# Performance work log

Hardware: AMD Instinct MI355X
Metric: run time of the kernel (lower is better)

Reference implementation:

```python
import jax, jax.numpy as jnp
import numpy as np

E, TOP, C, H, W, B = 8, 2, 128, 96, 96, 8
NUM_GATES = 4
KH = 3  # capsule conv kernel


def setup_inputs() -> dict:
    key = jax.random.key(0)
    ks = jax.random.split(key, 6)
    x = jax.random.normal(ks[0], (B, C, H, W), jnp.float32)
    # xavier_uniform for gates: bound = sqrt(6/(fan_in+fan_out))
    bound = float(np.sqrt(6.0 / (C + E)))
    G = jax.random.uniform(ks[1], (NUM_GATES, C, E), jnp.float32, -bound, bound)
    # per-expert capsule convs: the 16 parallel (C->capsule_dim) 3x3 convs are
    # stacked along the output-channel axis into one (C->C) conv per expert
    Wc = jax.random.normal(ks[2], (E, C, C, KH, KH), jnp.float32) * (1.0 / np.sqrt(C * KH * KH))
    bc = jax.random.normal(ks[3], (E, C), jnp.float32) * 0.01
    # 1x1 output projection per expert
    Wp = jax.random.normal(ks[4], (E, C, C), jnp.float32) * (1.0 / np.sqrt(C))
    bp = jax.random.normal(ks[5], (E, C), jnp.float32) * 0.01
    return {"x": x, "G": G, "Wc": Wc, "bc": bc, "Wp": Wp, "bp": bp}


def _squash(u):
    # squash over the full channel dim (dim=1), matching the torch module
    sn = jnp.sum(u * u, axis=1, keepdims=True)
    return (sn / (1.0 + sn)) * u / jnp.sqrt(sn + 1e-8)


def _expert(x, wc, bc, wp, bp):
    u = jax.lax.conv_general_dilated(
        x, wc, window_strides=(1, 1), padding='SAME',
        dimension_numbers=('NCHW', 'OIHW', 'NCHW')) + bc[None, :, None, None]
    u = jax.nn.relu(u)
    u = _squash(u)
    return jnp.einsum('bchw,oc->bohw', u, wp) + bp[None, :, None, None]


def _cv_squared(v):
    v = v.astype(jnp.float32)
    return jnp.var(v, ddof=1) / (jnp.mean(v) ** 2 + 1e-10)


def reference(x, G, Wc, bc, Wp, bp):
    Bn = x.shape[0]
    # run every expert on the full batch (dense equivalent of the masked dispatch)
    y_all = jax.vmap(lambda wc_, bc_, wp_, bp_: _expert(x, wc_, bc_, wp_, bp_))(
        Wc, bc, Wp, bp)  # [E, B, C, H, W]
    x_gap = jnp.mean(x, axis=(2, 3))  # [B, C]  (adaptive avg pool to 1x1)
    ys, losses = [], []
    for g in range(NUM_GATES):
        probs = jax.nn.softmax(x_gap @ G[g], axis=1)           # [B, E]
        tv, ti = jax.lax.top_k(probs, TOP)                     # [B, TOP]
        tw = jax.nn.softmax(tv, axis=1)                        # renormalized top-k weights
        out = jnp.zeros_like(x)
        for k in range(TOP):
            y_sel = y_all[ti[:, k], jnp.arange(Bn)]            # gather per-sample expert out
            out = out + y_sel * tw[:, k][:, None, None, None]
        ys.append(out)
        losses.append(_cv_squared(jnp.sum(probs, axis=0)))     # cv^2 of expert usage
    total_loss = jnp.mean(jnp.stack(losses))
    return (*ys, total_loss)
```

## Files before the change

kernel.cpp:

```cpp
#include <hip/hip_runtime.h>
#include <math.h>

#define CHW 9216
#define OPG 9437184

typedef unsigned short u16;
typedef __attribute__((ext_vector_type(8))) short short8;
typedef __attribute__((ext_vector_type(4))) float f32x4;

#define WS_XT  8192
#define WS_AT  18882560
#define WS_WPT 21241856

__device__ __forceinline__ u16 f2bf(float f) {
    unsigned u = __float_as_uint(f);
    u += 0x7fff + ((u >> 16) & 1);
    return (u16)(u >> 16);
}

__device__ __forceinline__ void gload_lds16(const void* g, void* l) {
    __builtin_amdgcn_global_load_lds(
        (const __attribute__((address_space(1))) void*)g,
        (__attribute__((address_space(3))) void*)l, 16, 0, 0);
}

__global__ void gap_kernel(const float* __restrict__ x, float* __restrict__ xgap) {
    int bc = blockIdx.x;
    const float* p = x + (size_t)bc * CHW;
    float s = 0.f;
    for (int i = threadIdx.x; i < CHW; i += 256) s += p[i];
    __shared__ float red[256];
    red[threadIdx.x] = s;
    __syncthreads();
    for (int off = 128; off > 0; off >>= 1) {
        if (threadIdx.x < off) red[threadIdx.x] += red[threadIdx.x + off];
        __syncthreads();
    }
    if (threadIdx.x == 0) xgap[bc] = red[0] * (1.0f / 9216.0f);
}

__global__ void gate_kernel(const float* __restrict__ G, float* __restrict__ ws,
                            float* __restrict__ loss_out) {
    __shared__ float gap_s[1024];
    __shared__ float logits[64];
    __shared__ float probs[64];
    __shared__ float vsum[8];
    __shared__ float losses[4];
    int t = threadIdx.x;
    for (int i = t; i < 1024; i += 64) gap_s[i] = ws[i];
    int b = t >> 3, e = t & 7;
    int* iw = (int*)(ws + 1344);
    float* wt = ws + 1408;
    __syncthreads();
    for (int g = 0; g < 4; ++g) {
        float acc = 0.f;
        const float* Gg = G + g * 1024;
        for (int c = 0; c < 128; ++c) acc += gap_s[b * 128 + c] * Gg[c * 8 + e];
        logits[t] = acc;
        __syncthreads();
        float m = -1e30f;
        for (int j = 0; j < 8; ++j) m = fmaxf(m, logits[b * 8 + j]);
        float den = 0.f;
        for (int j = 0; j < 8; ++j) den += expf(logits[b * 8 + j] - m);
        float pr = expf(acc - m) / den;
        probs[t] = pr;
        __syncthreads();
        if (e == 0) {
            int i0 = 0; float v0 = probs[b * 8];
            for (int j = 1; j < 8; ++j) { float v = probs[b * 8 + j]; if (v > v0) { v0 = v; i0 = j; } }
            int i1 = -1; float v1 = -1e30f;
            for (int j = 0; j < 8; ++j) { if (j == i0) continue; float v = probs[b * 8 + j]; if (v > v1) { v1 = v; i1 = j; } }
            float r = expf(v1 - v0);
            float inv = 1.f / (1.f + r);
            iw[g * 16 + b * 2 + 0] = i0;
            iw[g * 16 + b * 2 + 1] = i1;
            wt[g * 16 + b * 2 + 0] = inv;
            wt[g * 16 + b * 2 + 1] = r * inv;
        }
        if (t < 8) {
            float v = 0.f;
            for (int bb = 0; bb < 8; ++bb) v += probs[bb * 8 + t];
            vsum[t] = v;
        }
        __syncthreads();
        if (t == 0) {
            float mean = 0.f;
            for (int j = 0; j < 8; ++j) mean += vsum[j];
            mean *= 0.125f;
            float var = 0.f;
            for (int j = 0; j < 8; ++j) { float d = vsum[j] - mean; var += d * d; }
            var *= (1.f / 7.f);
            losses[g] = var / (mean * mean + 1e-10f);
        }
        __syncthreads();
    }
    if (t == 0) loss_out[0] = 0.25f * (losses[0] + losses[1] + losses[2] + losses[3]);
}

__global__ void pre_x(const float* __restrict__ x, u16* __restrict__ Xt) {
    int h = blockIdx.x, b = blockIdx.y, t = threadIdx.x;
    __shared__ u16 lds[12288];
    const float* xb = x + ((size_t)b * 128) * CHW + h * 96;
    for (int i = t; i < 12288; i += 256) {
        int c = i / 96, w = i - c * 96;
        lds[(c >> 6) * 6144 + w * 64 + ((c & 63) ^ ((w & 7) << 3))] = f2bf(xb[(size_t)c * CHW + w]);
    }
    __syncthreads();
    const unsigned* l32 = (const unsigned*)lds;
    unsigned* o32 = (unsigned*)Xt;
    for (int i = t; i < 6144; i += 256) {
        int hf = (i >= 3072) ? 1 : 0;
        int rem = i - hf * 3072;
        o32[((size_t)(b * 2 + hf) * 96 + h) * 3072 + rem] = l32[i];
    }
}

__global__ void pre_wc2(const float* __restrict__ Wc, u16* __restrict__ At2) {
    int idx = blockIdx.x * 256 + threadIdx.x;
    int s = idx & 7;
    int lane = (idx >> 3) & 63;
    int mb = (idx >> 9) & 3;
    int mi = (idx >> 11) & 1;
    int ck = (idx >> 12) & 1;
    int rem = idx >> 13;
    int r = rem % 9;
    int rem2 = rem / 9;
    int hf = rem2 & 1;
    int e = rem2 >> 1;
    int l15 = lane & 15, quad = lane >> 4;
    int o = mi * 64 + mb * 16 + l15;
    int cin = hf * 64 + ck * 32 + quad * 8 + s;
    size_t src = (((size_t)e * 128 + o) * 128 + cin) * 9 + r;
    At2[idx] = f2bf(Wc[src]);
}

__global__ void pre_wp(const float* __restrict__ Wp, u16* __restrict__ Wpt) {
    int i = blockIdx.x * 256 + threadIdx.x;
    if (i < 131072) Wpt[i] = f2bf(Wp[i]);
}

__launch_bounds__(512, 2)
__global__ void expert_kernel(const u16* __restrict__ Xt, const u16* __restrict__ At2,
                              const u16* __restrict__ Wpt,
                              const float* __restrict__ bc, const float* __restrict__ bp,
                              const float* __restrict__ ws, float* __restrict__ out) {
    int hs = blockIdx.x, b = blockIdx.y, g = blockIdx.z;
    int h0 = hs * 2;
    int t = threadIdx.x, lane = t & 63, wv = t >> 6;
    int mi = wv & 1, ni = wv >> 1;
    int l15 = lane & 15, quad = lane >> 4, q8 = quad * 8;
    int nrow = ni >> 1;
    int ncb = (ni & 1) * 48;

    const int* iw = (const int*)(ws + 1344);
    const float* wt = ws + 1408;
    int ee[2];
    float wwt[2];
    ee[0] = iw[g * 16 + b * 2 + 0]; ee[1] = iw[g * 16 + b * 2 + 1];
    wwt[0] = wt[g * 16 + b * 2 + 0]; wwt[1] = wt[g * 16 + b * 2 + 1];

    __shared__ __align__(16) char smem[115712];
    u16* Hs = (u16*)smem;
    float* part_s = (float*)smem;
    u16* v_s = (u16*)(smem + 9216);

    f32x4 zero = {0.f, 0.f, 0.f, 0.f};
    f32x4 acc[2][12];
    #pragma unroll
    for (int i = 0; i < 12; ++i) { acc[0][i] = zero; acc[1][i] = zero; }

    const u16* Ab0 = At2 + (size_t)(ee[0] * 2) * 73728;
    const u16* Ab1 = At2 + (size_t)(ee[1] * 2) * 73728;

    #define ASRC(P, U) ((P) + ((U) >= 18 ? 73728 + ((U) - 18) * 4096 : (U) * 4096))
    #define STAGE(U) { u16* ab_ = (u16*)(smem + 50176 + ((U) & 3) * 16384);          \
                       gload_lds16(ASRC(Ab0, (U)) + t * 8, ab_ + t * 8);             \
                       gload_lds16(ASRC(Ab1, (U)) + t * 8, ab_ + 4096 + t * 8); }

    {
        uint4 z; z.x = z.y = z.z = z.w = 0u;
        #pragma unroll
        for (int rr = 0; rr < 4; ++rr) {
            int row = h0 - 1 + rr;
            if (row < 0 || row >= 96)
                for (int i = t; i < 784; i += 512) *(uint4*)(Hs + rr * 6272 + i * 8) = z;
        }
        if (t < 64) {
            int rr = t >> 4, cs = (t >> 3) & 1, p = t & 7;
            *(uint4*)(Hs + rr * 6272 + cs * 97 * 64 + p * 8) = z;
        }
        const u16* Xb = Xt + (size_t)(b * 2 + 0) * 96 * 6144;
        #pragma unroll
        for (int rr = 0; rr < 4; ++rr) {
            int row = h0 - 1 + rr;
            if (row >= 0 && row < 96) {
                const u16* src = Xb + (size_t)row * 6144;
                u16* dst = Hs + rr * 6272 + 64;
                for (int i = t; i < 768; i += 512) gload_lds16(src + i * 8, dst + i * 8);
            }
        }
    }
    STAGE(0); STAGE(1);
    __syncthreads();

    #pragma unroll
    for (int u = 0; u < 36; ++u) {
        if (u == 18) {
            __builtin_amdgcn_s_barrier();
            const u16* Xb = Xt + (size_t)(b * 2 + 1) * 96 * 6144;
            #pragma unroll
            for (int rr = 0; rr < 4; ++rr) {
                int row = h0 - 1 + rr;
                if (row >= 0 && row < 96) {
                    const u16* src = Xb + (size_t)row * 6144;
                    u16* dst = Hs + rr * 6272 + 64;
                    for (int i = t; i < 768; i += 512) gload_lds16(src + i * 8, dst + i * 8);
                }
            }
        }
        if (u <= 33) STAGE(u + 2);
        if (u == 18 || u == 35) asm volatile("s_waitcnt vmcnt(0)" ::: "memory");
        else if (u == 34)       asm volatile("s_waitcnt vmcnt(2)" ::: "memory");
        else                    asm volatile("s_waitcnt vmcnt(4)" ::: "memory");
        __builtin_amdgcn_s_barrier();

        int s = (u >= 18) ? u - 18 : u;
        int r = s >> 1, ck = s & 1;
        int dyi = r / 3, dxi = r - dyi * 3;
        const u16* ab = (const u16*)(smem + 50176 + (u & 3) * 16384);

        short8 af0[4], af1[4], bv[3];
        #pragma unroll
        for (int mb = 0; mb < 4; ++mb) {
            af0[mb] = *(const short8*)(ab + mi * 2048 + mb * 512 + lane * 8);
            af1[mb] = *(const short8*)(ab + 4096 + mi * 2048 + mb * 512 + lane * 8);
        }
        int hb = (nrow + dyi) * 12544;
        #pragma unroll
        for (int j = 0; j < 3; ++j) {
            int col = ncb + j * 16 + l15 + dxi;
            int ba = hb + col * 128 + ((q8 ^ (((col - 1) & 7) << 3)) << 1);
            bv[j] = *(const short8*)(smem + (ba ^ (ck << 6)));
        }
        __builtin_amdgcn_s_setprio(1);
        #pragma unroll
        for (int mb = 0; mb < 4; ++mb)
            #pragma unroll
            for (int j = 0; j < 3; ++j) {
                acc[0][mb * 3 + j] = __builtin_amdgcn_mfma_f32_16x16x32_bf16(af0[mb], bv[j], acc[0][mb * 3 + j], 0, 0, 0);
                acc[1][mb * 3 + j] = __builtin_amdgcn_mfma_f32_16x16x32_bf16(af1[mb], bv[j], acc[1][mb * 3 + j], 0, 0, 0);
            }
        __builtin_amdgcn_s_setprio(0);
    }
    #undef STAGE
    #undef ASRC

    #pragma unroll
    for (int xp = 0; xp < 2; ++xp) {
        int e_ = ee[xp];
        __syncthreads();
        #pragma unroll
        for (int j = 0; j < 3; ++j) {
            int n = ni * 48 + j * 16 + l15;
            float ssum = 0.f;
            #pragma unroll
            for (int mb = 0; mb < 4; ++mb) {
                f32x4 a = acc[xp][mb * 3 + j];
                #pragma unroll
                for (int rg = 0; rg < 4; ++rg) {
                    float u = fmaxf(a[rg] + bc[e_ * 128 + mi * 64 + mb * 16 + quad * 4 + rg], 0.f);
                    a[rg] = u; ssum += u * u;
                }
                acc[xp][mb * 3 + j] = a;
            }
            part_s[n * 12 + mi * 4 + quad] = ssum;
        }
        __syncthreads();
        #pragma unroll
        for (int j = 0; j < 3; ++j) {
            int n = ni * 48 + j * 16 + l15;
            f32x4 p0 = *(const f32x4*)(part_s + n * 12);
            f32x4 p1 = *(const f32x4*)(part_s + n * 12 + 4);
            float sn2 = p0[0] + p0[1] + p0[2] + p0[3] + p1[0] + p1[1] + p1[2] + p1[3];
            float fsj = sn2 / ((1.f + sn2) * sqrtf(sn2 + 1e-8f));
            int sw = (n & 7) << 3;
            #pragma unroll
            for (int mb = 0; mb < 4; ++mb) {
                f32x4 a = acc[xp][mb * 3 + j];
                short4 pk;
                pk.x = (short)f2bf(a[0] * fsj); pk.y = (short)f2bf(a[1] * fsj);
                pk.z = (short)f2bf(a[2] * fsj); pk.w = (short)f2bf(a[3] * fsj);
                int cb = mb * 16 + quad * 4;
                *(short4*)(v_s + n * 128 + ((cb ^ sw) | (mi << 6))) = pk;
            }
        }
        __syncthreads();
        #pragma unroll
        for (int i = 0; i < 12; ++i) acc[xp][i] = zero;
        const u16* We_ = Wpt + (size_t)e_ * 16384;
        #pragma unroll
        for (int kk = 0; kk < 4; ++kk) {
            short8 af[4];
            #pragma unroll
            for (int mb = 0; mb < 4; ++mb)
                af[mb] = *(const short8*)(We_ + (mi * 64 + mb * 16 + l15) * 128 + kk * 32 + q8);
            short8 bvv[3];
            #pragma unroll
            for (int j = 0; j < 3; ++j) {
                int n = ni * 48 + j * 16 + l15;
                int sw = (n & 7) << 3;
                int pos = ((kk & 2) << 5) | ((((kk & 1) << 5) + q8) ^ sw);
                bvv[j] = *(const short8*)(v_s + n * 128 + pos);
            }
            #pragma unroll
            for (int mb = 0; mb < 4; ++mb)
                #pragma unroll
                for (int j = 0; j < 3; ++j)
                    acc[xp][mb * 3 + j] = __builtin_amdgcn_mfma_f32_16x16x32_bf16(af[mb], bvv[j], acc[xp][mb * 3 + j], 0, 0, 0);
        }
    }

    int row = h0 + nrow;
    #pragma unroll
    for (int mb = 0; mb < 4; ++mb)
        #pragma unroll
        for (int rg = 0; rg < 4; ++rg) {
            int o = mi * 64 + mb * 16 + quad * 4 + rg;
            float y0b = bp[ee[0] * 128 + o];
            float y1b = bp[ee[1] * 128 + o];
            size_t obase = (size_t)g * OPG + ((size_t)(b * 128 + o)) * CHW + (size_t)row * 96;
            #pragma unroll
            for (int j = 0; j < 3; ++j) {
                float y0 = acc[0][mb * 3 + j][rg] + y0b;
                float y1 = acc[1][mb * 3 + j][rg] + y1b;
                out[obase + ncb + j * 16 + l15] = wwt[0] * y0 + wwt[1] * y1;
            }
        }
}

extern "C" void kernel_launch(void* const* d_in, const int* in_sizes, int n_in,
                              void* d_out, int out_size, void* d_ws, size_t ws_size,
                              hipStream_t stream) {
    const float* x  = (const float*)d_in[0];
    const float* G  = (const float*)d_in[1];
    const float* Wc = (const float*)d_in[2];
    const float* bc = (const float*)d_in[3];
    const float* Wp = (const float*)d_in[4];
    const float* bp = (const float*)d_in[5];
    float* out = (float*)d_out;
    float* ws  = (float*)d_ws;
    u16* Xt  = (u16*)((char*)d_ws + WS_XT);
    u16* At2 = (u16*)((char*)d_ws + WS_AT);
    u16* Wpt = (u16*)((char*)d_ws + WS_WPT);

    gap_kernel<<<dim3(1024), dim3(256), 0, stream>>>(x, ws);
    gate_kernel<<<dim3(1), dim3(64), 0, stream>>>(G, ws, out + (size_t)4 * OPG);
    pre_x<<<dim3(96, 8), dim3(256), 0, stream>>>(x, Xt);
    pre_wc2<<<dim3(4608), dim3(256), 0, stream>>>(Wc, At2);
    pre_wp<<<dim3(512), dim3(256), 0, stream>>>(Wp, Wpt);
    expert_kernel<<<dim3(48, 8, 4), dim3(512), 0, stream>>>(Xt, At2, Wpt, bc, bp, ws, out);
}
```

Before: 429.7 us.

## Prefetch A fragments into registers one step ahead with triple-buffered LDS

Cuts the LDS staging ring for expert weight tiles from four buffers to three. Each step now loads the next step's A fragments into a double-buffered register array, so the MFMAs use fragments already held in registers. Synchronisation moves to a full vmcnt(0) wait plus barrier at the end of every iteration. The aim is to hide LDS read latency behind MFMA work, at the cost of more VGPRs and less in-flight global-load depth, since the wait now drains all loads each step.

```diff
diff --git a/kernel.cpp b/kernel.cpp
--- a/kernel.cpp
+++ b/kernel.cpp
@@ -159,7 +159,7 @@
     ee[0] = iw[g * 16 + b * 2 + 0]; ee[1] = iw[g * 16 + b * 2 + 1];
     wwt[0] = wt[g * 16 + b * 2 + 0]; wwt[1] = wt[g * 16 + b * 2 + 1];
 
-    __shared__ __align__(16) char smem[115712];
+    __shared__ __align__(16) char smem[99328];
     u16* Hs = (u16*)smem;
     float* part_s = (float*)smem;
     u16* v_s = (u16*)(smem + 9216);
@@ -169,11 +169,13 @@
     #pragma unroll
     for (int i = 0; i < 12; ++i) { acc[0][i] = zero; acc[1][i] = zero; }
 
+    int abase = mi * 2048 + lane * 8;
+
     const u16* Ab0 = At2 + (size_t)(ee[0] * 2) * 73728;
     const u16* Ab1 = At2 + (size_t)(ee[1] * 2) * 73728;
 
     #define ASRC(P, U) ((P) + ((U) >= 18 ? 73728 + ((U) - 18) * 4096 : (U) * 4096))
-    #define STAGE(U) { u16* ab_ = (u16*)(smem + 50176 + ((U) & 3) * 16384);          \
+    #define STAGE(U) { u16* ab_ = (u16*)(smem + 50176 + ((U) % 3) * 16384);          \
                        gload_lds16(ASRC(Ab0, (U)) + t * 8, ab_ + t * 8);             \
                        gload_lds16(ASRC(Ab1, (U)) + t * 8, ab_ + 4096 + t * 8); }
 
@@ -203,10 +205,19 @@
     STAGE(0); STAGE(1);
     __syncthreads();
 
+    short8 afr[2][2][4];
+    {
+        const u16* ab = (const u16*)(smem + 50176);
+        #pragma unroll
+        for (int mb = 0; mb < 4; ++mb) {
+            afr[0][0][mb] = *(const short8*)(ab + abase + mb * 512);
+            afr[0][1][mb] = *(const short8*)(ab + 4096 + abase + mb * 512);
+        }
+    }
+
     #pragma unroll
     for (int u = 0; u < 36; ++u) {
         if (u == 18) {
-            __builtin_amdgcn_s_barrier();
             const u16* Xb = Xt + (size_t)(b * 2 + 1) * 96 * 6144;
             #pragma unroll
             for (int rr = 0; rr < 4; ++rr) {
@@ -217,40 +228,42 @@
                     for (int i = t; i < 768; i += 512) gload_lds16(src + i * 8, dst + i * 8);
                 }
             }
-        }
-        if (u <= 33) STAGE(u + 2);
-        if (u == 18 || u == 35) asm volatile("s_waitcnt vmcnt(0)" ::: "memory");
-        else if (u == 34)       asm volatile("s_waitcnt vmcnt(2)" ::: "memory");
-        else                    asm volatile("s_waitcnt vmcnt(4)" ::: "memory");
-        __builtin_amdgcn_s_barrier();
+            asm volatile("s_waitcnt vmcnt(0)" ::: "memory");
+            __builtin_amdgcn_s_barrier();
+        }
+        if (u < 34) STAGE(u + 2);
 
         int s = (u >= 18) ? u - 18 : u;
         int r = s >> 1, ck = s & 1;
         int dyi = r / 3, dxi = r - dyi * 3;
-        const u16* ab = (const u16*)(smem + 50176 + (u & 3) * 16384);
-
-        short8 af0[4], af1[4], bv[3];
-        #pragma unroll
-        for (int mb = 0; mb < 4; ++mb) {
-            af0[mb] = *(const short8*)(ab + mi * 2048 + mb * 512 + lane * 8);
-            af1[mb] = *(const short8*)(ab + 4096 + mi * 2048 + mb * 512 + lane * 8);
-        }
         int hb = (nrow + dyi) * 12544;
+
+        short8 bv[3];
         #pragma unroll
         for (int j = 0; j < 3; ++j) {
             int col = ncb + j * 16 + l15 + dxi;
             int ba = hb + col * 128 + ((q8 ^ (((col - 1) & 7) << 3)) << 1);
             bv[j] = *(const short8*)(smem + (ba ^ (ck << 6)));
         }
+        if (u < 35) {
+            const u16* ab = (const u16*)(smem + 50176 + ((u + 1) % 3) * 16384);
+            #pragma unroll
+            for (int mb = 0; mb < 4; ++mb) {
+                afr[(u + 1) & 1][0][mb] = *(const short8*)(ab + abase + mb * 512);
+                afr[(u + 1) & 1][1][mb] = *(const short8*)(ab + 4096 + abase + mb * 512);
+            }
+        }
         __builtin_amdgcn_s_setprio(1);
         #pragma unroll
         for (int mb = 0; mb < 4; ++mb)
             #pragma unroll
             for (int j = 0; j < 3; ++j) {
-                acc[0][mb * 3 + j] = __builtin_amdgcn_mfma_f32_16x16x32_bf16(af0[mb], bv[j], acc[0][mb * 3 + j], 0, 0, 0);
-                acc[1][mb * 3 + j] = __builtin_amdgcn_mfma_f32_16x16x32_bf16(af1[mb], bv[j], acc[1][mb * 3 + j], 0, 0, 0);
+                acc[0][mb * 3 + j] = __builtin_amdgcn_mfma_f32_16x16x32_bf16(afr[u & 1][0][mb], bv[j], acc[0][mb * 3 + j], 0, 0, 0);
+                acc[1][mb * 3 + j] = __builtin_amdgcn_mfma_f32_16x16x32_bf16(afr[u & 1][1][mb], bv[j], acc[1][mb * 3 + j], 0, 0, 0);
             }
         __builtin_amdgcn_s_setprio(0);
+        asm volatile("s_waitcnt vmcnt(0)" ::: "memory");
+        __builtin_amdgcn_s_barrier();
     }
     #undef STAGE
     #undef ASRC
```

After: 450.5 us. 1.05x slower.

## Software-pipeline LDS fragment reads with MFMA in conv main loop, triple-buffer A

Applied to the files above, without the earlier changes.

Restructures the 36-step conv K loop into two halves with register double-buffered B fragments and split A fragment reads. Reads for the next step are interleaved between the two expert MFMA groups. The A staging ring shrinks from four to three LDS buffers, cutting shared memory use. The intent is to hide LDS read latency behind MFMA work and possibly raise occupancy, at the cost of more registers and two barriers per step. Each step also waits on vmcnt(0) for global loads.

```diff
diff --git a/kernel.cpp b/kernel.cpp
--- a/kernel.cpp
+++ b/kernel.cpp
@@ -159,7 +159,7 @@
     ee[0] = iw[g * 16 + b * 2 + 0]; ee[1] = iw[g * 16 + b * 2 + 1];
     wwt[0] = wt[g * 16 + b * 2 + 0]; wwt[1] = wt[g * 16 + b * 2 + 1];
 
-    __shared__ __align__(16) char smem[115712];
+    __shared__ __align__(16) char smem[99328];
     u16* Hs = (u16*)smem;
     float* part_s = (float*)smem;
     u16* v_s = (u16*)(smem + 9216);
@@ -169,13 +169,26 @@
     #pragma unroll
     for (int i = 0; i < 12; ++i) { acc[0][i] = zero; acc[1][i] = zero; }
 
+    int abase = mi * 2048 + lane * 8;
+
     const u16* Ab0 = At2 + (size_t)(ee[0] * 2) * 73728;
     const u16* Ab1 = At2 + (size_t)(ee[1] * 2) * 73728;
 
     #define ASRC(P, U) ((P) + ((U) >= 18 ? 73728 + ((U) - 18) * 4096 : (U) * 4096))
-    #define STAGE(U) { u16* ab_ = (u16*)(smem + 50176 + ((U) & 3) * 16384);          \
+    #define STAGE(U) { u16* ab_ = (u16*)(smem + 50176 + ((U) % 3) * 16384);          \
                        gload_lds16(ASRC(Ab0, (U)) + t * 8, ab_ + t * 8);             \
                        gload_lds16(ASRC(Ab1, (U)) + t * 8, ab_ + 4096 + t * 8); }
+    #define RD_AF(DST, G, XOFF) { const u16* abr_ = (const u16*)(smem + 50176 + ((G) % 3) * 16384) + (XOFF); \
+        _Pragma("unroll") for (int mb_ = 0; mb_ < 4; ++mb_) DST[mb_] = *(const short8*)(abr_ + abase + mb_ * 512); }
+    #define RD_BV(DST, G) { const int s_ = (G) % 18, r_ = s_ >> 1, ck_ = s_ & 1;     \
+        const int dyi_ = r_ / 3, dxi_ = r_ - dyi_ * 3, hb_ = (nrow + dyi_) * 12544;  \
+        _Pragma("unroll") for (int j_ = 0; j_ < 3; ++j_) {                           \
+            int col_ = ncb + j_ * 16 + l15 + dxi_;                                   \
+            int ba_ = hb_ + col_ * 128 + ((q8 ^ (((col_ - 1) & 7) << 3)) << 1);      \
+            DST[j_] = *(const short8*)(smem + (ba_ ^ (ck_ << 6))); } }
+    #define MFMA12(XP, AF, BV) { _Pragma("unroll") for (int mb_ = 0; mb_ < 4; ++mb_) \
+        _Pragma("unroll") for (int j_ = 0; j_ < 3; ++j_)                             \
+            acc[XP][mb_ * 3 + j_] = __builtin_amdgcn_mfma_f32_16x16x32_bf16(AF[mb_], BV[j_], acc[XP][mb_ * 3 + j_], 0, 0, 0); }
 
     {
         uint4 z; z.x = z.y = z.z = z.w = 0u;
@@ -203,10 +216,11 @@
     STAGE(0); STAGE(1);
     __syncthreads();
 
+    short8 af0[4], af1[4], bvA[3], bvB[3];
+
     #pragma unroll
-    for (int u = 0; u < 36; ++u) {
-        if (u == 18) {
-            __builtin_amdgcn_s_barrier();
+    for (int hf = 0; hf < 2; ++hf) {
+        if (hf == 1) {
             const u16* Xb = Xt + (size_t)(b * 2 + 1) * 96 * 6144;
             #pragma unroll
             for (int rr = 0; rr < 4; ++rr) {
@@ -217,43 +231,38 @@
                     for (int i = t; i < 768; i += 512) gload_lds16(src + i * 8, dst + i * 8);
                 }
             }
-        }
-        if (u <= 33) STAGE(u + 2);
-        if (u == 18 || u == 35) asm volatile("s_waitcnt vmcnt(0)" ::: "memory");
-        else if (u == 34)       asm volatile("s_waitcnt vmcnt(2)" ::: "memory");
-        else                    asm volatile("s_waitcnt vmcnt(4)" ::: "memory");
-        __builtin_amdgcn_s_barrier();
-
-        int s = (u >= 18) ? u - 18 : u;
-        int r = s >> 1, ck = s & 1;
-        int dyi = r / 3, dxi = r - dyi * 3;
-        const u16* ab = (const u16*)(smem + 50176 + (u & 3) * 16384);
-
-        short8 af0[4], af1[4], bv[3];
-        #pragma unroll
-        for (int mb = 0; mb < 4; ++mb) {
-            af0[mb] = *(const short8*)(ab + mi * 2048 + mb * 512 + lane * 8);
-            af1[mb] = *(const short8*)(ab + 4096 + mi * 2048 + mb * 512 + lane * 8);
-        }
-        int hb = (nrow + dyi) * 12544;
-        #pragma unroll
-        for (int j = 0; j < 3; ++j) {
-            int col = ncb + j * 16 + l15 + dxi;
-            int ba = hb + col * 128 + ((q8 ^ (((col - 1) & 7) << 3)) << 1);
-            bv[j] = *(const short8*)(smem + (ba ^ (ck << 6)));
-        }
-        __builtin_amdgcn_s_setprio(1);
-        #pragma unroll
-        for (int mb = 0; mb < 4; ++mb)
-            #pragma unroll
-            for (int j = 0; j < 3; ++j) {
-                acc[0][mb * 3 + j] = __builtin_amdgcn_mfma_f32_16x16x32_bf16(af0[mb], bv[j], acc[0][mb * 3 + j], 0, 0, 0);
-                acc[1][mb * 3 + j] = __builtin_amdgcn_mfma_f32_16x16x32_bf16(af1[mb], bv[j], acc[1][mb * 3 + j], 0, 0, 0);
-            }
-        __builtin_amdgcn_s_setprio(0);
+            asm volatile("s_waitcnt vmcnt(0)" ::: "memory");
+            __builtin_amdgcn_s_barrier();
+        }
+        RD_AF(af0, hf * 18, 0);
+        RD_BV(bvA, hf * 18);
+
+        #pragma unroll
+        for (int u = 0; u < 18; ++u) {
+            const int gg = hf * 18 + u;
+            if (gg + 2 <= 35) STAGE(gg + 2);
+            RD_AF(af1, gg, 4096);
+            __builtin_amdgcn_s_setprio(1);
+            if (u & 1) { MFMA12(0, af0, bvB); } else { MFMA12(0, af0, bvA); }
+            __builtin_amdgcn_s_setprio(0);
+            __builtin_amdgcn_s_barrier();
+            if (u < 17) {
+                if (u & 1) { RD_BV(bvA, gg + 1); } else { RD_BV(bvB, gg + 1); }
+                RD_AF(af0, gg + 1, 0);
+            }
+            __builtin_amdgcn_s_setprio(1);
+            if (u & 1) { MFMA12(1, af1, bvB); } else { MFMA12(1, af1, bvA); }
+            __builtin_amdgcn_s_setprio(0);
+            asm volatile("s_waitcnt vmcnt(0)" ::: "memory");
+            if (u == 17) asm volatile("s_waitcnt lgkmcnt(0)" ::: "memory");
+            __builtin_amdgcn_s_barrier();
+        }
     }
     #undef STAGE
     #undef ASRC
+    #undef RD_AF
+    #undef RD_BV
+    #undef MFMA12
 
     #pragma unroll
     for (int xp = 0; xp < 2; ++xp) {
```

Measured after the change: 430.2 us. No clear change (+0.1%).
